# Kernel tuning notes

Measured on AMD Instinct MI355X. Metric: run time of the kernel, lower is better.

Reference implementation:

```python
import jax, jax.numpy as jnp
import numpy as np

B, S, HID, NH, HD = 2, 2048, 768, 12, 64
WINDOW = 128           # ModernBERT local attention window
ROPE_THETA = 10000.0   # local_rope_theta (layer_index=0 -> is_local_attention=True)


def _rotate_half(x):
    x1, x2 = jnp.split(x, 2, axis=-1)
    return jnp.concatenate([-x2, x1], axis=-1)


def setup_inputs() -> dict:
    key = jax.random.key(0)
    k1, k2, k3 = jax.random.split(key, 3)
    hidden_embed = jax.random.normal(k1, (B, S, HID), dtype=jnp.float32)
    Wq = jax.random.normal(k2, (HID, HID), dtype=jnp.float32) * (HID ** -0.5)
    Wo = jax.random.normal(k3, (HID, HID), dtype=jnp.float32) * (HID ** -0.5)
    position_index = jnp.arange(S, dtype=jnp.int32).reshape(1, S)
    # sliding-window additive mask: 0 inside window, -inf outside
    i = jnp.arange(S)
    dist = jnp.abs(i[:, None] - i[None, :])
    local_attention_mask = jnp.where(dist <= WINDOW // 2, 0.0, -jnp.inf).astype(jnp.float32)[None, None]
    global_attention_mask = jnp.zeros((1, 1, S, S), dtype=jnp.float32)
    return {
        "hidden_embed": hidden_embed,
        "Wq": Wq,
        "Wo": Wo,
        "local_attention_mask": local_attention_mask,
        "global_attention_mask": global_attention_mask,
        "position_index": position_index,
    }


def reference(hidden_embed, Wq, Wo, local_attention_mask, global_attention_mask, position_index):
    # q projection; NOTE: source has k = q.view(...), v = q.view(...) -> k and v ARE q
    q = hidden_embed @ Wq.T                                  # [B,S,HID]
    q = q.reshape(B, S, NH, HD).transpose(0, 2, 1, 3)        # [B,NH,S,HD]

    # RoPE
    inv_freq = 1.0 / (ROPE_THETA ** (jnp.arange(0, HD, 2, dtype=jnp.float32) / HD))  # [HD/2]
    pos = position_index.reshape(-1).astype(jnp.float32)     # [S]
    freqs = pos[:, None] * inv_freq[None, :]                 # [S,HD/2]
    emb = jnp.concatenate([freqs, freqs], axis=-1)           # [S,HD]
    cos, sin = jnp.cos(emb), jnp.sin(emb)
    q_rot = q * cos + _rotate_half(q) * sin                  # [B,NH,S,HD]
    k_rot = q_rot                                            # k == q before rope -> same after rope
    v = q                                                    # v == q (no rope on v)

    # masked SDPA (local layer -> local sliding-window mask)
    scale = jnp.asarray(HD, jnp.float32) ** -0.5
    scores = jnp.einsum('bhtd,bhsd->bhts', q_rot, k_rot) * scale + local_attention_mask
    attn = jax.nn.softmax(scores, axis=-1)                   # [B,NH,S,S]
    out = jnp.einsum('bhts,bhsd->bhtd', attn, v)             # [B,NH,S,HD]
    out = out.transpose(0, 2, 1, 3).reshape(B, S, HID)
    return out @ Wo.T
```

## Files before the change

kernel.cpp:

```cpp
#include <hip/hip_runtime.h>
#include <hip/hip_bf16.h>
#include <math.h>
#include <stdint.h>

#define B_    2
#define S_    2048
#define HID_  768
#define NH_   12
#define HD_   64
#define NROWS (B_ * S_)
#define N_HID_ELEM (NROWS * HID_)
#define N_W_ELEM   (HID_ * HID_)

#define KW   224
#define KSTR 232

typedef __bf16 bf16x8 __attribute__((ext_vector_type(8)));
typedef float  floatx4 __attribute__((ext_vector_type(4)));

__global__ void convert_inputs_kernel(const float* __restrict__ src_hidden,
                                      const float* __restrict__ src_w1,
                                      const float* __restrict__ src_w2,
                                      __hip_bfloat16* __restrict__ Hb,
                                      __hip_bfloat16* __restrict__ Wqb,
                                      __hip_bfloat16* __restrict__ Wob)
{
    int i = blockIdx.x * blockDim.x + threadIdx.x;
    const float* src;
    __hip_bfloat16* dst;
    int off;
    const int NH4 = N_HID_ELEM / 4, NW4 = N_W_ELEM / 4;
    if (i < NH4)           { src = src_hidden; dst = Hb;  off = i; }
    else if (i < NH4+NW4)  { src = src_w1;     dst = Wqb; off = i - NH4; }
    else if (i < NH4+2*NW4){ src = src_w2;     dst = Wob; off = i - NH4 - NW4; }
    else return;
    float4 v = reinterpret_cast<const float4*>(src)[off];
    __hip_bfloat16 o[4] = { __float2bfloat16(v.x), __float2bfloat16(v.y),
                            __float2bfloat16(v.z), __float2bfloat16(v.w) };
    *reinterpret_cast<uint64_t*>(dst + 4 * (size_t)off) = *reinterpret_cast<uint64_t*>(o);
}

__device__ __forceinline__ void gload_lds16(const __hip_bfloat16* g, __hip_bfloat16* l)
{
    __builtin_amdgcn_global_load_lds(
        (const __attribute__((address_space(1))) void*)g,
        (__attribute__((address_space(3))) void*)l, 16, 0, 0);
}

template<int MODE>
__global__ __launch_bounds__(256) void gemm128(
    const __hip_bfloat16* __restrict__ A,
    const __hip_bfloat16* __restrict__ W,
    __hip_bfloat16* __restrict__ C,
    __hip_bfloat16* __restrict__ C2,
    float* __restrict__ Cf,
    const int* __restrict__ pos_idx,
    int M, int N, int K)
{
    __shared__ __align__(16) __hip_bfloat16 Alds[128 * 32];
    __shared__ __align__(16) __hip_bfloat16 Wlds[128 * 32];

    const int tid  = threadIdx.x;
    const int wv   = tid >> 6;
    const int lane = tid & 63;
    const int l16  = lane & 15;
    const int quad = lane >> 4;
    const int m0 = blockIdx.x * 128;
    const int n0 = blockIdx.y * 128;
    const int wm = (wv >> 1) * 64;
    const int wn = (wv & 1) * 64;

    const int c_lane = wv * 64 + lane;
    const int row0 = c_lane >> 2, col80 = (c_lane & 3) * 8;
    const int row1 = (c_lane + 256) >> 2, col81 = ((c_lane + 256) & 3) * 8;

    const __hip_bfloat16* gA0 = A + (size_t)(m0 + row0) * K + col80;
    const __hip_bfloat16* gA1 = A + (size_t)(m0 + row1) * K + col81;
    const __hip_bfloat16* gW0 = W + (size_t)(n0 + row0) * K + col80;
    const __hip_bfloat16* gW1 = W + (size_t)(n0 + row1) * K + col81;
    __hip_bfloat16* lA0 = &Alds[(wv * 64) * 8];
    __hip_bfloat16* lA1 = &Alds[(wv * 64 + 256) * 8];
    __hip_bfloat16* lW0 = &Wlds[(wv * 64) * 8];
    __hip_bfloat16* lW1 = &Wlds[(wv * 64 + 256) * 8];

    floatx4 acc[4][4] = {};

    for (int k0 = 0; k0 < K; k0 += 32) {
        gload_lds16(gA0 + k0, lA0);
        gload_lds16(gA1 + k0, lA1);
        gload_lds16(gW0 + k0, lW0);
        gload_lds16(gW1 + k0, lW1);
        __syncthreads();

        bf16x8 af[4], bf[4];
#pragma unroll
        for (int t = 0; t < 4; ++t)
            af[t] = *reinterpret_cast<const bf16x8*>(&Alds[(wm + t * 16 + l16) * 32 + quad * 8]);
#pragma unroll
        for (int u = 0; u < 4; ++u)
            bf[u] = *reinterpret_cast<const bf16x8*>(&Wlds[(wn + u * 16 + l16) * 32 + quad * 8]);
#pragma unroll
        for (int t = 0; t < 4; ++t)
#pragma unroll
            for (int u = 0; u < 4; ++u)
                acc[t][u] = __builtin_amdgcn_mfma_f32_16x16x32_bf16(af[t], bf[u], acc[t][u], 0, 0, 0);
        __syncthreads();
    }

    if (MODE == 1) {
        const int nbase = n0 + wn;
#pragma unroll
        for (int t = 0; t < 4; ++t) {
#pragma unroll
            for (int r = 0; r < 4; ++r) {
                int m = m0 + wm + t * 16 + quad * 4 + r;
                int s = m & (S_ - 1);
                float pos = (float)pos_idx[s];
#pragma unroll
                for (int u = 0; u < 2; ++u) {
                    float f = (float)(u * 16 + l16);
                    float inv = exp2f(f * (-0.41524101186092024f));
                    float sn, cs;
                    sincosf(pos * inv, &sn, &cs);
                    float q0 = acc[t][u][r];
                    float q1 = acc[t][u + 2][r];
                    size_t base = (size_t)m * HID_ + nbase + u * 16 + l16;
                    C [base]      = __float2bfloat16(q0);
                    C [base + 32] = __float2bfloat16(q1);
                    C2[base]      = __float2bfloat16(q0 * cs - q1 * sn);
                    C2[base + 32] = __float2bfloat16(q1 * cs + q0 * sn);
                }
            }
        }
    } else {
#pragma unroll
        for (int t = 0; t < 4; ++t)
#pragma unroll
            for (int u = 0; u < 4; ++u)
#pragma unroll
                for (int r = 0; r < 4; ++r) {
                    int row = m0 + wm + t * 16 + quad * 4 + r;
                    int col = n0 + wn + u * 16 + l16;
                    Cf[(size_t)row * N + col] = acc[t][u][r];
                }
    }
}

__global__ __launch_bounds__(256) void attn_kernel(
    const __hip_bfloat16* __restrict__ Q,
    const __hip_bfloat16* __restrict__ Qr,
    __hip_bfloat16* __restrict__ O)
{
    __shared__ __align__(16) __hip_bfloat16 Vt[64][KSTR];
    __shared__ __align__(16) __hip_bfloat16 Pl[64][KSTR];

    const int bh = blockIdx.y;
    const int b  = bh / NH_;
    const int h  = bh % NH_;
    const int i0 = blockIdx.x * 64;
    const int tid = threadIdx.x;

    for (int idx = tid; idx < KW * 64; idx += 256) {
        int w = idx >> 6;
        int d = idx & 63;
        int j = i0 - 64 + w;
        int jc = min(max(j, 0), S_ - 1);
        Vt[d][w] = Q[((size_t)(b * S_ + jc)) * HID_ + h * HD_ + d];
    }
    __syncthreads();

    const int wv   = tid >> 6;
    const int lane = tid & 63;
    const int l16  = lane & 15;
    const int quad = lane >> 4;

    floatx4 sc[10] = {};
    const __hip_bfloat16* qrow =
        Qr + ((size_t)(b * S_ + i0 + wv * 16 + l16)) * HID_ + h * HD_ + quad * 8;
#pragma unroll
    for (int ks = 0; ks < 2; ++ks) {
        bf16x8 a = *reinterpret_cast<const bf16x8*>(qrow + ks * 32);
#pragma unroll
        for (int t = 0; t < 10; ++t) {
            int j = i0 - 64 + (wv + t) * 16 + l16;
            int jc = min(max(j, 0), S_ - 1);
            bf16x8 bfr = *reinterpret_cast<const bf16x8*>(
                Qr + ((size_t)(b * S_ + jc)) * HID_ + h * HD_ + ks * 32 + quad * 8);
            sc[t] = __builtin_amdgcn_mfma_f32_16x16x32_bf16(a, bfr, sc[t], 0, 0, 0);
        }
    }

    const float scale = 0.125f;
    float denom[4];
#pragma unroll
    for (int r = 0; r < 4; ++r) {
        const int R = wv * 16 + quad * 4 + r;
        float xv[10];
        float mx = -3.0e38f;
#pragma unroll
        for (int t = 0; t < 10; ++t) {
            int w = (wv + t) * 16 + l16;
            int j = i0 - 64 + w;
            bool valid = (w >= R) && (w <= R + 128) && (j >= 0) && (j < S_);
            float x = valid ? sc[t][r] * scale : -1.0e30f;
            xv[t] = x;
            mx = fmaxf(mx, x);
        }
#pragma unroll
        for (int msk = 1; msk < 16; msk <<= 1) mx = fmaxf(mx, __shfl_xor(mx, msk, 64));
        float sum = 0.f;
#pragma unroll
        for (int t = 0; t < 10; ++t) {
            float p = __expf(xv[t] - mx);
            sum += p;
            Pl[R][(wv + t) * 16 + l16] = __float2bfloat16(p);
        }
#pragma unroll
        for (int msk = 1; msk < 16; msk <<= 1) sum += __shfl_xor(sum, msk, 64);
        denom[r] = sum;
    }
    __syncthreads();

    floatx4 oacc[4] = {};
#pragma unroll
    for (int c = 0; c < 5; ++c) {
        const int base = wv * 16 + c * 32;
        bf16x8 a = *reinterpret_cast<const bf16x8*>(&Pl[wv * 16 + l16][base + quad * 8]);
#pragma unroll
        for (int u = 0; u < 4; ++u) {
            bf16x8 bfr = *reinterpret_cast<const bf16x8*>(&Vt[u * 16 + l16][base + quad * 8]);
            oacc[u] = __builtin_amdgcn_mfma_f32_16x16x32_bf16(a, bfr, oacc[u], 0, 0, 0);
        }
    }

#pragma unroll
    for (int u = 0; u < 4; ++u)
#pragma unroll
        for (int r = 0; r < 4; ++r) {
            int row = i0 + wv * 16 + quad * 4 + r;
            int col = u * 16 + l16;
            O[((size_t)(b * S_ + row)) * HID_ + h * HD_ + col] =
                __float2bfloat16(oacc[u][r] / denom[r]);
        }
}

extern "C" void kernel_launch(void* const* d_in, const int* in_sizes, int n_in,
                              void* d_out, int out_size, void* d_ws, size_t ws_size,
                              hipStream_t stream)
{
    int ih = -1, iw1 = -1, iw2 = -1, ip = -1;
    for (int i = 0; i < n_in; ++i) {
        int s = in_sizes[i];
        if      (s == N_HID_ELEM && ih < 0) ih = i;
        else if (s == N_W_ELEM)  { if (iw1 < 0) iw1 = i; else if (iw2 < 0) iw2 = i; }
        else if (s == S_ && ip < 0) ip = i;
    }
    if (ih < 0)  ih = 0;
    if (iw1 < 0) iw1 = 1;
    if (iw2 < 0) iw2 = 2;
    if (ip < 0)  ip = 5;

    const float* hidden = (const float*)d_in[ih];
    const float* w1     = (const float*)d_in[iw1];
    const float* w2     = (const float*)d_in[iw2];
    const int*   pos    = (const int*)d_in[ip];

    __hip_bfloat16* Hb  = (__hip_bfloat16*)d_ws;
    __hip_bfloat16* Wqb = Hb  + N_HID_ELEM;
    __hip_bfloat16* Wob = Wqb + N_W_ELEM;
    __hip_bfloat16* Q   = Wob + N_W_ELEM;
    __hip_bfloat16* Qr  = Q   + N_HID_ELEM;
    __hip_bfloat16* AO  = Hb;

    int conv4 = (N_HID_ELEM + 2 * N_W_ELEM) / 4;
    convert_inputs_kernel<<<(conv4 + 255) / 256, 256, 0, stream>>>(
        hidden, w1, w2, Hb, Wqb, Wob);

    dim3 gblk(NROWS / 128, HID_ / 128);

    gemm128<1><<<gblk, 256, 0, stream>>>(Hb, Wqb, Q, Qr, nullptr, pos,
                                         NROWS, HID_, HID_);

    attn_kernel<<<dim3(S_ / 64, B_ * NH_), 256, 0, stream>>>(Q, Qr, AO);

    gemm128<2><<<gblk, 256, 0, stream>>>(AO, Wob, nullptr, nullptr, (float*)d_out,
                                         nullptr, NROWS, HID_, HID_);
}
```

Before: 163.1 us.

## Shrink GEMM tiles to 64x64 with XOR-swizzled LDS and K-step 64

Both projection GEMMs move from 128x128 tiles with K-step 32 to 64x64 tiles with K-step 64. Each wave now computes a 16x64 strip. The LDS layout uses an XOR swizzle of 16-byte chunks to avoid bank conflicts on fragment reads. The grid grows from 192 to 768 blocks so the 256 CUs are better filled, at the cost of less register-level reuse per block and more global traffic per FLOP.

```diff
diff --git a/kernel.cpp b/kernel.cpp
--- a/kernel.cpp
+++ b/kernel.cpp
@@ -48,7 +48,7 @@
 }
 
 template<int MODE>
-__global__ __launch_bounds__(256) void gemm128(
+__global__ __launch_bounds__(256) void gemm64(
     const __hip_bfloat16* __restrict__ A,
     const __hip_bfloat16* __restrict__ W,
     __hip_bfloat16* __restrict__ C,
@@ -57,92 +57,87 @@
     const int* __restrict__ pos_idx,
     int M, int N, int K)
 {
-    __shared__ __align__(16) __hip_bfloat16 Alds[128 * 32];
-    __shared__ __align__(16) __hip_bfloat16 Wlds[128 * 32];
+    __shared__ __align__(16) __hip_bfloat16 Alds[64 * 64];
+    __shared__ __align__(16) __hip_bfloat16 Wlds[64 * 64];
 
     const int tid  = threadIdx.x;
     const int wv   = tid >> 6;
     const int lane = tid & 63;
     const int l16  = lane & 15;
     const int quad = lane >> 4;
-    const int m0 = blockIdx.x * 128;
-    const int n0 = blockIdx.y * 128;
-    const int wm = (wv >> 1) * 64;
-    const int wn = (wv & 1) * 64;
-
-    const int c_lane = wv * 64 + lane;
-    const int row0 = c_lane >> 2, col80 = (c_lane & 3) * 8;
-    const int row1 = (c_lane + 256) >> 2, col81 = ((c_lane + 256) & 3) * 8;
-
-    const __hip_bfloat16* gA0 = A + (size_t)(m0 + row0) * K + col80;
-    const __hip_bfloat16* gA1 = A + (size_t)(m0 + row1) * K + col81;
-    const __hip_bfloat16* gW0 = W + (size_t)(n0 + row0) * K + col80;
-    const __hip_bfloat16* gW1 = W + (size_t)(n0 + row1) * K + col81;
+    const int m0 = blockIdx.x * 64;
+    const int n0 = blockIdx.y * 64;
+
+    const int c0 = wv * 64 + lane;
+    const int c1 = c0 + 256;
+    const int r0 = c0 >> 3, k0c = ((c0 & 7) ^ (r0 & 7)) * 8;
+    const int r1 = c1 >> 3, k1c = ((c1 & 7) ^ (r1 & 7)) * 8;
+
+    const __hip_bfloat16* gA0 = A + (size_t)(m0 + r0) * K + k0c;
+    const __hip_bfloat16* gA1 = A + (size_t)(m0 + r1) * K + k1c;
+    const __hip_bfloat16* gW0 = W + (size_t)(n0 + r0) * K + k0c;
+    const __hip_bfloat16* gW1 = W + (size_t)(n0 + r1) * K + k1c;
     __hip_bfloat16* lA0 = &Alds[(wv * 64) * 8];
     __hip_bfloat16* lA1 = &Alds[(wv * 64 + 256) * 8];
     __hip_bfloat16* lW0 = &Wlds[(wv * 64) * 8];
     __hip_bfloat16* lW1 = &Wlds[(wv * 64 + 256) * 8];
 
-    floatx4 acc[4][4] = {};
-
-    for (int k0 = 0; k0 < K; k0 += 32) {
+    floatx4 acc[4] = {};
+    const int ra = wv * 16 + l16;
+
+    for (int k0 = 0; k0 < K; k0 += 64) {
         gload_lds16(gA0 + k0, lA0);
         gload_lds16(gA1 + k0, lA1);
         gload_lds16(gW0 + k0, lW0);
         gload_lds16(gW1 + k0, lW1);
         __syncthreads();
 
-        bf16x8 af[4], bf[4];
-#pragma unroll
-        for (int t = 0; t < 4; ++t)
-            af[t] = *reinterpret_cast<const bf16x8*>(&Alds[(wm + t * 16 + l16) * 32 + quad * 8]);
+#pragma unroll
+        for (int ks = 0; ks < 2; ++ks) {
+            const int kc = ks * 4 + quad;
+            bf16x8 a = *reinterpret_cast<const bf16x8*>(
+                &Alds[ra * 64 + ((kc ^ (ra & 7)) * 8)]);
+#pragma unroll
+            for (int u = 0; u < 4; ++u) {
+                const int rw = u * 16 + l16;
+                bf16x8 w = *reinterpret_cast<const bf16x8*>(
+                    &Wlds[rw * 64 + ((kc ^ (rw & 7)) * 8)]);
+                acc[u] = __builtin_amdgcn_mfma_f32_16x16x32_bf16(a, w, acc[u], 0, 0, 0);
+            }
+        }
+        __syncthreads();
+    }
+
+    if (MODE == 1) {
+#pragma unroll
+        for (int r = 0; r < 4; ++r) {
+            int m = m0 + wv * 16 + quad * 4 + r;
+            int s = m & (S_ - 1);
+            float pos = (float)pos_idx[s];
+#pragma unroll
+            for (int u = 0; u < 2; ++u) {
+                float f = (float)(u * 16 + l16);
+                float inv = exp2f(f * (-0.41524101186092024f));
+                float sn, cs;
+                sincosf(pos * inv, &sn, &cs);
+                float q0 = acc[u][r];
+                float q1 = acc[u + 2][r];
+                size_t base = (size_t)m * HID_ + n0 + u * 16 + l16;
+                C [base]      = __float2bfloat16(q0);
+                C [base + 32] = __float2bfloat16(q1);
+                C2[base]      = __float2bfloat16(q0 * cs - q1 * sn);
+                C2[base + 32] = __float2bfloat16(q1 * cs + q0 * sn);
+            }
+        }
+    } else {
 #pragma unroll
         for (int u = 0; u < 4; ++u)
-            bf[u] = *reinterpret_cast<const bf16x8*>(&Wlds[(wn + u * 16 + l16) * 32 + quad * 8]);
-#pragma unroll
-        for (int t = 0; t < 4; ++t)
-#pragma unroll
-            for (int u = 0; u < 4; ++u)
-                acc[t][u] = __builtin_amdgcn_mfma_f32_16x16x32_bf16(af[t], bf[u], acc[t][u], 0, 0, 0);
-        __syncthreads();
-    }
-
-    if (MODE == 1) {
-        const int nbase = n0 + wn;
-#pragma unroll
-        for (int t = 0; t < 4; ++t) {
 #pragma unroll
             for (int r = 0; r < 4; ++r) {
-                int m = m0 + wm + t * 16 + quad * 4 + r;
-                int s = m & (S_ - 1);
-                float pos = (float)pos_idx[s];
-#pragma unroll
-                for (int u = 0; u < 2; ++u) {
-                    float f = (float)(u * 16 + l16);
-                    float inv = exp2f(f * (-0.41524101186092024f));
-                    float sn, cs;
-                    sincosf(pos * inv, &sn, &cs);
-                    float q0 = acc[t][u][r];
-                    float q1 = acc[t][u + 2][r];
-                    size_t base = (size_t)m * HID_ + nbase + u * 16 + l16;
-                    C [base]      = __float2bfloat16(q0);
-                    C [base + 32] = __float2bfloat16(q1);
-                    C2[base]      = __float2bfloat16(q0 * cs - q1 * sn);
-                    C2[base + 32] = __float2bfloat16(q1 * cs + q0 * sn);
-                }
+                int row = m0 + wv * 16 + quad * 4 + r;
+                int col = n0 + u * 16 + l16;
+                Cf[(size_t)row * N + col] = acc[u][r];
             }
-        }
-    } else {
-#pragma unroll
-        for (int t = 0; t < 4; ++t)
-#pragma unroll
-            for (int u = 0; u < 4; ++u)
-#pragma unroll
-                for (int r = 0; r < 4; ++r) {
-                    int row = m0 + wm + t * 16 + quad * 4 + r;
-                    int col = n0 + wn + u * 16 + l16;
-                    Cf[(size_t)row * N + col] = acc[t][u][r];
-                }
     }
 }
 
@@ -276,13 +271,13 @@
     convert_inputs_kernel<<<(conv4 + 255) / 256, 256, 0, stream>>>(
         hidden, w1, w2, Hb, Wqb, Wob);
 
-    dim3 gblk(NROWS / 128, HID_ / 128);
-
-    gemm128<1><<<gblk, 256, 0, stream>>>(Hb, Wqb, Q, Qr, nullptr, pos,
-                                         NROWS, HID_, HID_);
+    dim3 gblk(NROWS / 64, HID_ / 64);
+
+    gemm64<1><<<gblk, 256, 0, stream>>>(Hb, Wqb, Q, Qr, nullptr, pos,
+                                        NROWS, HID_, HID_);
 
     attn_kernel<<<dim3(S_ / 64, B_ * NH_), 256, 0, stream>>>(Q, Qr, AO);
 
-    gemm128<2><<<gblk, 256, 0, stream>>>(AO, Wob, nullptr, nullptr, (float*)d_out,
-                                         nullptr, NROWS, HID_, HID_);
-}
+    gemm64<2><<<gblk, 256, 0, stream>>>(AO, Wob, nullptr, nullptr, (float*)d_out,
+                                        nullptr, NROWS, HID_, HID_);
+}
```

Measured after the change: 146.2 us. 10.4% less time.
